# Optimization experiments

Measured on AMD Instinct MI355X. Metric: run time of the kernel, lower is better.

The kernel has to match this reference:

```python
import jax, jax.numpy as jnp
import numpy as np

B, S, D = 1, 4096, 896
NH, NKV, HD = 14, 2, 64
ROPE_BASE = 1000000.0

def rotate_half(x):
    x1, x2 = x[..., :x.shape[-1] // 2], x[..., x.shape[-1] // 2:]
    return jnp.concatenate((-x2, x1), axis=-1)

def rope_tables(seq_len, head_dim, base):
    inv_freq = 1.0 / (base ** (jnp.arange(0, head_dim, 2, dtype=jnp.float32) / head_dim))
    t = jnp.arange(seq_len, dtype=jnp.float32)
    freqs = jnp.einsum('i,j->ij', t, inv_freq)
    emb = jnp.concatenate((freqs, freqs), axis=-1)  # [S, HD]
    return jnp.cos(emb), jnp.sin(emb)

def setup_inputs() -> dict:
    key = jax.random.key(0)
    ks = jax.random.split(key, 6)
    hidden_states = jax.random.normal(ks[0], (B, S, D), dtype=jnp.float32)
    # additive causal mask [1,1,S,S]
    neg = jnp.finfo(jnp.float32).min
    causal = jnp.where(jnp.tril(jnp.ones((S, S), dtype=bool)), 0.0, neg)
    attention_mask = causal[None, None, :, :].astype(jnp.float32)
    sc = 0.02
    Wq = jax.random.normal(ks[1], (D, NH * HD), dtype=jnp.float32) * sc
    Wk = jax.random.normal(ks[2], (D, NKV * HD), dtype=jnp.float32) * sc
    Wv = jax.random.normal(ks[3], (D, NKV * HD), dtype=jnp.float32) * sc
    Wo = jax.random.normal(ks[4], (D, D), dtype=jnp.float32) * sc
    bq = jnp.zeros((NH * HD,), jnp.float32)
    bk = jnp.zeros((NKV * HD,), jnp.float32)
    bv = jnp.zeros((NKV * HD,), jnp.float32)
    return {"hidden_states": hidden_states, "attention_mask": attention_mask,
            "Wq": Wq, "bq": bq, "Wk": Wk, "bk": bk, "Wv": Wv, "bv": bv, "Wo": Wo}

def reference(hidden_states, attention_mask, Wq, bq, Wk, bk, Wv, bv, Wo):
    b, s, _ = hidden_states.shape
    groups = NH // NKV
    q = (hidden_states @ Wq + bq).reshape(b, s, NH, HD)
    k = (hidden_states @ Wk + bk).reshape(b, s, NKV, HD)
    v = (hidden_states @ Wv + bv).reshape(b, s, NKV, HD)
    cos, sin = rope_tables(s, HD, ROPE_BASE)
    cos = cos[None, :, None, :]
    sin = sin[None, :, None, :]
    q = q * cos + rotate_half(q) * sin
    k = k * cos + rotate_half(k) * sin
    # GQA: repeat KV heads
    k = jnp.repeat(k, groups, axis=2)
    v = jnp.repeat(v, groups, axis=2)
    # [b, h, s, d]
    q = jnp.transpose(q, (0, 2, 1, 3))
    k = jnp.transpose(k, (0, 2, 1, 3))
    v = jnp.transpose(v, (0, 2, 1, 3))
    attn = jnp.einsum('bhqd,bhkd->bhqk', q, k) / jnp.sqrt(jnp.float32(HD))
    attn = attn + attention_mask
    attn = jax.nn.softmax(attn, axis=-1)
    out = jnp.einsum('bhqk,bhkd->bhqd', attn, v)
    out = jnp.transpose(out, (0, 2, 1, 3)).reshape(b, s, NH * HD)
    return out @ Wo
```

## Files before the change

### kernel.cpp

```cpp
#include <hip/hip_runtime.h>
#include <math.h>

constexpr int S_    = 4096;
constexpr int Dm    = 896;
constexpr int NHd   = 14;
constexpr int NKVh  = 2;
constexpr int HDim  = 64;
constexpr int NQ    = NHd * HDim;
constexpr int NK    = NKVh * HDim;
constexpr int NQK   = NQ + NK;
constexpr int GROUPS = NHd / NKVh;
constexpr float L2B   = 19.9315685693241740873f;
constexpr float LOG2E = 1.44269504088896340736f;

constexpr int NUNITS = 952;

typedef __attribute__((ext_vector_type(8)))  short bf16x8;
typedef __attribute__((ext_vector_type(4)))  short bf16x4;
typedef __attribute__((ext_vector_type(4)))  float f32x4;
typedef __attribute__((ext_vector_type(16))) float f32x16;
typedef __attribute__((ext_vector_type(4)))  int   i32x4;

__device__ __forceinline__ short f2bf(float f) {
  unsigned u = __builtin_bit_cast(unsigned, f);
  unsigned r = (u + 0x7FFFu + ((u >> 16) & 1u)) >> 16;
  return (short)r;
}
__device__ __forceinline__ float bf2f(short s) {
  return __builtin_bit_cast(float, ((unsigned)(unsigned short)s) << 16);
}

__device__ __forceinline__ unsigned cvtpk(float lo, float hi) {
  unsigned r;
  asm("v_cvt_pk_bf16_f32 %0, %1, %2" : "=v"(r) : "v"(lo), "v"(hi));
  return r;
}

__device__ __forceinline__ void gload16(const void* g, void* l) {
  __builtin_amdgcn_global_load_lds(
      (const __attribute__((address_space(1))) unsigned int*)g,
      (__attribute__((address_space(3))) unsigned int*)l, 16, 0, 0);
}

__global__ __launch_bounds__(256) void prep_all(
    const float* __restrict__ hs, short* __restrict__ hsb,
    float* __restrict__ cost, float* __restrict__ sint,
    const float* __restrict__ Wq, const float* __restrict__ Wk,
    const float* __restrict__ Wv, const float* __restrict__ Wo,
    short* __restrict__ wtq, short* __restrict__ wto)
{
  const int bid = blockIdx.x;
  const int tid = threadIdx.x;
  if (bid < 1792) {
    int idx = bid * 256 + tid;
    float4 a = ((const float4*)hs)[idx * 2];
    float4 b = ((const float4*)hs)[idx * 2 + 1];
    bf16x8 o;
    o[0] = f2bf(a.x); o[1] = f2bf(a.y); o[2] = f2bf(a.z); o[3] = f2bf(a.w);
    o[4] = f2bf(b.x); o[5] = f2bf(b.y); o[6] = f2bf(b.z); o[7] = f2bf(b.w);
    ((bf16x8*)hsb)[idx] = o;
    return;
  }
  if (bid < 2304) {
    int idx = (bid - 1792) * 256 + tid;
    int m = idx >> 5, j = idx & 31;
    float invf = exp2f(-(float)j * (L2B / 32.0f));
    float th = (float)m * invf;
    float s, c;
    sincosf(th, &s, &c);
    cost[idx] = c;
    sint[idx] = s;
    return;
  }
  __shared__ float t[64 * 68];
  const int b2 = bid - 2304;
  const int kt = b2 % 14;
  const int by = b2 / 14;

  const float* src; int srcN, nt; short* dst; int rowOff;
  if (by < 14)      { src = Wq; srcN = NQ; nt = by;      dst = wtq; rowOff = 0; }
  else if (by < 16) { src = Wk; srcN = NK; nt = by - 14; dst = wtq; rowOff = 896; }
  else if (by < 18) { src = Wv; srcN = NK; nt = by - 16; dst = wtq; rowOff = 1024; }
  else              { src = Wo; srcN = NQ; nt = by - 18; dst = wto; rowOff = 0; }

  #pragma unroll
  for (int i = 0; i < 4; i++) {
    int idx = tid + i * 256;
    int r = idx >> 4, c4 = (idx & 15) * 4;
    *(float4*)&t[r * 68 + c4] =
        *(const float4*)&src[(size_t)(kt * 64 + r) * srcN + nt * 64 + c4];
  }
  __syncthreads();
  const int nl = tid >> 2;
  const int kc = (tid & 3) * 16;
  bf16x8 o0, o1;
  #pragma unroll
  for (int i = 0; i < 8; i++) o0[i] = f2bf(t[(kc + i) * 68 + nl]);
  #pragma unroll
  for (int i = 0; i < 8; i++) o1[i] = f2bf(t[(kc + 8 + i) * 68 + nl]);
  short* dp = dst + (size_t)(rowOff + nt * 64 + nl) * 896 + kt * 64 + kc;
  *(bf16x8*)dp = o0;
  *(bf16x8*)(dp + 8) = o1;
}

template<int EPI>
__global__ __launch_bounds__(256) void gemm64(
    const short* __restrict__ A, const short* __restrict__ Bt,
    const float* __restrict__ biasq, const float* __restrict__ biask,
    const float* __restrict__ biasv,
    const float* __restrict__ cost, const float* __restrict__ sint,
    short* __restrict__ qkb, short* __restrict__ vtb,
    float* __restrict__ outp)
{
  __shared__ short Als[64 * 64];
  __shared__ short Bls[128 * 64];
  const int tid = threadIdx.x;
  const int lane = tid & 63;
  const int w = tid >> 6;
  const int wm = w >> 1, wn = w & 1;
  const int r16 = lane & 15, rg = lane >> 4;
  const int bm = blockIdx.x, bn = blockIdx.y;

  const f32x4 zero4 = {0.f, 0.f, 0.f, 0.f};
  f32x4 acc[2][4];
  #pragma unroll
  for (int mt = 0; mt < 2; mt++)
    #pragma unroll
    for (int nt = 0; nt < 4; nt++) acc[mt][nt] = zero4;

  const int srow = (lane >> 3);
  const int scol = (lane & 7) * 8;

  for (int kt = 0; kt < 14; ++kt) {
    __syncthreads();
    #pragma unroll
    for (int i = 0; i < 2; i++) {
      int c = w * 2 + i;
      int row = c * 8 + srow;
      gload16(A + (size_t)(bm * 64 + row) * 896 + kt * 64 + scol, &Als[c * 512]);
    }
    #pragma unroll
    for (int i = 0; i < 4; i++) {
      int c = w * 4 + i;
      int row = c * 8 + srow;
      gload16(Bt + (size_t)(bn * 128 + row) * 896 + kt * 64 + scol, &Bls[c * 512]);
    }
    __syncthreads();

    bf16x8 af[2][2], bfr[4][2];
    #pragma unroll
    for (int mt = 0; mt < 2; mt++)
      #pragma unroll
      for (int ks = 0; ks < 2; ks++)
        af[mt][ks] = *(const bf16x8*)&Als[(wm * 32 + mt * 16 + r16) * 64 + ks * 32 + rg * 8];
    #pragma unroll
    for (int nt = 0; nt < 4; nt++)
      #pragma unroll
      for (int ks = 0; ks < 2; ks++)
        bfr[nt][ks] = *(const bf16x8*)&Bls[(wn * 64 + nt * 16 + r16) * 64 + ks * 32 + rg * 8];
    #pragma unroll
    for (int mt = 0; mt < 2; mt++)
      #pragma unroll
      for (int nt = 0; nt < 4; nt++)
        #pragma unroll
        for (int ks = 0; ks < 2; ks++)
          acc[mt][nt] = __builtin_amdgcn_mfma_f32_16x16x32_bf16(
              af[mt][ks], bfr[nt][ks], acc[mt][nt], 0, 0, 0);
  }

  if (EPI == 0) {
    const int nbase = bn * 128 + wn * 64;
    if (bn < 8) {
      const float scl = (bn < 7) ? (0.125f * LOG2E) : 1.0f;
      const float* bias = (bn < 7) ? biasq : (biask - 896);
      #pragma unroll
      for (int mt = 0; mt < 2; mt++) {
        const int m0 = bm * 64 + wm * 32 + mt * 16 + rg * 4;
        #pragma unroll
        for (int nt = 0; nt < 4; nt++) {
          int n = nbase + nt * 16 + r16;
          int j = n & 31;
          float sgn = (n & 32) ? 1.f : -1.f;
          float b0 = bias[n], b1 = bias[n ^ 32];
          #pragma unroll
          for (int r = 0; r < 4; r++) {
            int m = m0 + r;
            float c_ = cost[m * 32 + j], s_ = sint[m * 32 + j];
            float val = ((acc[mt][nt][r] + b0) * c_ +
                         sgn * (acc[mt][nt ^ 2][r] + b1) * s_) * scl;
            qkb[(size_t)m * NQK + n] = f2bf(val);
          }
        }
      }
    } else {
      #pragma unroll
      for (int mt = 0; mt < 2; mt++) {
        const int m0 = bm * 64 + wm * 32 + mt * 16 + rg * 4;
        #pragma unroll
        for (int nt = 0; nt < 4; nt++) {
          int vc = wn * 64 + nt * 16 + r16;
          float b0 = biasv[vc];
          bf16x4 pk;
          #pragma unroll
          for (int r = 0; r < 4; r++) pk[r] = f2bf(acc[mt][nt][r] + b0);
          *(bf16x4*)&vtb[(size_t)vc * S_ + m0] = pk;
        }
      }
    }
  } else {
    #pragma unroll
    for (int mt = 0; mt < 2; mt++) {
      const int m0 = bm * 64 + wm * 32 + mt * 16 + rg * 4;
      #pragma unroll
      for (int nt = 0; nt < 4; nt++) {
        int n = bn * 128 + wn * 64 + nt * 16 + r16;
        #pragma unroll
        for (int r = 0; r < 4; r++)
          outp[(size_t)(m0 + r) * NQ + n] = acc[mt][nt][r];
      }
    }
  }
}

__global__ __launch_bounds__(256, 3) void flash_mfma(
    const short* __restrict__ qkb, const short* __restrict__ vtb,
    short* __restrict__ attnb, short* __restrict__ orec,
    float* __restrict__ mlrec, unsigned* __restrict__ cnt)
{
  __shared__ __align__(16) char lds[32768];
  __shared__ int s_unit;

  const int tid  = threadIdx.x;
  const int lane = tid & 63;
  const int w    = tid >> 6;
  const int q32  = lane & 31;
  const int hi   = lane >> 5;

  const int c8   = tid & 7;
  const int key0 = tid >> 3;
  const int key1 = key0 + 32;
  const int swz0 = (c8 ^ (key0 & 7)) << 4;
  const int swz1 = (c8 ^ (key1 & 7)) << 4;

  bf16x8 ones;
  #pragma unroll
  for (int j = 0; j < 8; j++) ones[j] = (short)0x3F80;

  for (;;) {
    __syncthreads();
    if (tid == 0) s_unit = (int)atomicAdd(cnt, 1u);
    __syncthreads();
    const int u = s_unit;
    if (u >= NUNITS) break;

    const int e = u / 14;
    const int h = u - e * 14;
    int qt, ci;
    if (e < 36)      { qt = 31 - e / 3; ci = e - (31 - qt) * 3; }
    else if (e < 60) { int f = e - 36; qt = 19 - (f >> 1); ci = f & 1; }
    else             { qt = 67 - e; ci = 0; }
    const int K  = 2 * (qt + 1);
    const int n  = (qt < 8) ? 1 : (qt < 20) ? 2 : 3;
    const int L  = (K + n - 1) / n;
    const int kt_lo = ci * L;
    const int kt_hi = (kt_lo + L < K) ? (kt_lo + L) : K;
    const int kv = h / GROUPS;
    const int q0 = qt * 128;
    const int kbase2 = (NQ + kv * HDim) * 2;
    const int qg = q0 + w * 32 + q32;

    bf16x8 qf[4];
    {
      const short* qp = qkb + (size_t)qg * NQK + h * HDim + hi * 8;
      #pragma unroll
      for (int ks = 0; ks < 4; ++ks) qf[ks] = *(const bf16x8*)(qp + ks * 16);
    }

    f32x16 acc_o[2], acc_l;
    float m_run = 0.f;
    #pragma unroll
    for (int r = 0; r < 16; ++r) { acc_o[0][r] = 0.f; acc_o[1][r] = 0.f; acc_l[r] = 0.f; }

    const char* ksrc0 = (const char*)qkb + (size_t)(kt_lo * 64 + key0) * 2048 + kbase2 + swz0;
    const char* ksrc1 = (const char*)qkb + (size_t)(kt_lo * 64 + key1) * 2048 + kbase2 + swz1;
    const char* vsrc0 = (const char*)vtb + (size_t)(kv * 64 + key0) * 8192 + (size_t)kt_lo * 128 + swz0;
    const char* vsrc1 = (const char*)vtb + (size_t)(kv * 64 + key1) * 8192 + (size_t)kt_lo * 128 + swz1;

    gload16(ksrc0, lds + w * 1024);
    gload16(ksrc1, lds + 4096 + w * 1024);
    gload16(vsrc0, lds + 8192 + w * 1024);
    gload16(vsrc1, lds + 12288 + w * 1024);
    ksrc0 += 131072; ksrc1 += 131072;
    vsrc0 += 128;    vsrc1 += 128;

    for (int kt = kt_lo; kt < kt_hi; ++kt) {
      const int cur = (kt - kt_lo) & 1;
      asm volatile("s_waitcnt vmcnt(0)" ::: "memory");
      __builtin_amdgcn_s_barrier();
      if (kt + 1 < kt_hi) {
        char* B = lds + ((cur ^ 1) << 14);
        gload16(ksrc0, B + w * 1024);
        gload16(ksrc1, B + 4096 + w * 1024);
        gload16(vsrc0, B + 8192 + w * 1024);
        gload16(vsrc1, B + 12288 + w * 1024);
        ksrc0 += 131072; ksrc1 += 131072;
        vsrc0 += 128;    vsrc1 += 128;
      }
      __builtin_amdgcn_sched_barrier(0);
      const char* KsB = lds + (cur << 14);
      const char* VtB = KsB + 8192;
      const int kb = kt * 64;

      f32x16 sc[2];
      #pragma unroll
      for (int r = 0; r < 16; ++r) { sc[0][r] = 0.f; sc[1][r] = 0.f; }
      #pragma unroll
      for (int t = 0; t < 2; ++t) {
        const int key = t * 32 + q32;
        #pragma unroll
        for (int ks = 0; ks < 4; ++ks) {
          bf16x8 kf = *(const bf16x8*)(KsB + key * 128 + (((2 * ks + hi) ^ (key & 7)) << 4));
          sc[t] = __builtin_amdgcn_mfma_f32_32x32x16_bf16(kf, qf[ks], sc[t], 0, 0, 0);
        }
      }

      if (kb + 63 > q0 + w * 32) {
        #pragma unroll
        for (int t = 0; t < 2; ++t)
          #pragma unroll
          for (int r = 0; r < 16; ++r) {
            int key = kb + t * 32 + (r & 3) + 8 * (r >> 2) + 4 * hi;
            sc[t][r] = (key > qg) ? -1e30f : sc[t][r];
          }
      }

      f32x16 mm;
      #pragma unroll
      for (int r = 0; r < 16; ++r) mm[r] = fmaxf(sc[0][r], sc[1][r]);
      #pragma unroll
      for (int r = 0; r < 8; ++r) mm[r] = fmaxf(mm[r], mm[r + 8]);
      #pragma unroll
      for (int r = 0; r < 4; ++r) mm[r] = fmaxf(mm[r], mm[r + 4]);
      float pm = fmaxf(fmaxf(mm[0], mm[1]), fmaxf(mm[2], mm[3]));
      {
        float a = pm, b = pm;
        asm("v_permlane32_swap_b32 %0, %1" : "+v"(a), "+v"(b));
        pm = fmaxf(a, b);
      }

      if (!__all(pm <= m_run + 8.0f)) {
        float newm = fmaxf(m_run, pm);
        float scl = exp2f(m_run - newm);
        m_run = newm;
        acc_l[0] *= scl;
        #pragma unroll
        for (int r = 0; r < 16; ++r) { acc_o[0][r] *= scl; acc_o[1][r] *= scl; }
      }

      #pragma unroll
      for (int t = 0; t < 2; ++t)
        #pragma unroll
        for (int r = 0; r < 16; ++r) sc[t][r] = exp2f(sc[t][r] - m_run);

      unsigned U0[2][4], U1[2][4];
      #pragma unroll
      for (int t = 0; t < 2; ++t)
        #pragma unroll
        for (int a = 0; a < 4; ++a) {
          U0[t][a] = cvtpk(sc[t][4 * a],     sc[t][4 * a + 1]);
          U1[t][a] = cvtpk(sc[t][4 * a + 2], sc[t][4 * a + 3]);
        }

      #pragma unroll
      for (int kp = 0; kp < 4; ++kp) {
        const int t = kp >> 1, c = kp & 1;
        unsigned x0 = U0[t][2 * c], y0 = U0[t][2 * c + 1];
        unsigned x1 = U1[t][2 * c], y1 = U1[t][2 * c + 1];
        asm("v_permlane32_swap_b32 %0, %1" : "+v"(x0), "+v"(y0));
        asm("v_permlane32_swap_b32 %0, %1" : "+v"(x1), "+v"(y1));
        i32x4 pi = {(int)x0, (int)x1, (int)y0, (int)y1};
        bf16x8 pf = __builtin_bit_cast(bf16x8, pi);
        acc_l = __builtin_amdgcn_mfma_f32_32x32x16_bf16(ones, pf, acc_l, 0, 0, 0);
        #pragma unroll
        for (int dt = 0; dt < 2; ++dt) {
          const int d = dt * 32 + q32;
          bf16x8 vf = *(const bf16x8*)(VtB + d * 128 + (((2 * kp + hi) ^ (d & 7)) << 4));
          acc_o[dt] = __builtin_amdgcn_mfma_f32_32x32x16_bf16(vf, pf, acc_o[dt], 0, 0, 0);
        }
      }
    }

    if (n == 1) {
      const float inv = 1.0f / acc_l[0];
      short* op = attnb + (size_t)qg * NQ + h * HDim + 4 * hi;
      #pragma unroll
      for (int dt = 0; dt < 2; ++dt)
        #pragma unroll
        for (int rq = 0; rq < 4; ++rq) {
          bf16x4 pk;
          pk[0] = f2bf(acc_o[dt][4 * rq]     * inv);
          pk[1] = f2bf(acc_o[dt][4 * rq + 1] * inv);
          pk[2] = f2bf(acc_o[dt][4 * rq + 2] * inv);
          pk[3] = f2bf(acc_o[dt][4 * rq + 3] * inv);
          *(bf16x4*)(op + dt * 32 + 8 * rq) = pk;
        }
    } else {
      const int qloc = w * 32 + q32;
      short* op;
      if (ci == 0) {
        op = attnb + (size_t)qg * NQ + h * HDim + 4 * hi;
      } else {
        int er = (qt < 20) ? (h * 36 + (qt - 8))
                           : (h * 36 + 12 + (qt - 20) * 2 + (ci - 1));
        op = orec + (size_t)er * 8192 + (size_t)qloc * 64 + 4 * hi;
      }
      #pragma unroll
      for (int dt = 0; dt < 2; ++dt)
        #pragma unroll
        for (int rq = 0; rq < 4; ++rq) {
          bf16x4 pk;
          pk[0] = f2bf(acc_o[dt][4 * rq]);
          pk[1] = f2bf(acc_o[dt][4 * rq + 1]);
          pk[2] = f2bf(acc_o[dt][4 * rq + 2]);
          pk[3] = f2bf(acc_o[dt][4 * rq + 3]);
          *(bf16x4*)(op + dt * 32 + 8 * rq) = pk;
        }
      if (hi == 0) {
        int co = (qt < 20) ? (8 + (qt - 8) * 2 + ci) : (32 + (qt - 20) * 3 + ci);
        float2 ml = {m_run, acc_l[0]};
        *(float2*)(mlrec + ((size_t)(h * 68 + co) * 128 + qloc) * 2) = ml;
      }
    }
  }
}

__global__ __launch_bounds__(128) void merge_chunks(
    const short* __restrict__ orec, const float* __restrict__ mlrec,
    short* __restrict__ attnb)
{
  const int b = blockIdx.x;
  const int h = b / 24;
  const int qt = 8 + (b - h * 24);
  const int n = (qt < 20) ? 2 : 3;
  const int qloc = threadIdx.x;
  const int q = qt * 128 + qloc;

  const int co0 = (qt < 20) ? (8 + (qt - 8) * 2) : (32 + (qt - 20) * 3);
  float2 ml0 = *(const float2*)(mlrec + ((size_t)(h * 68 + co0)     * 128 + qloc) * 2);
  float2 ml1 = *(const float2*)(mlrec + ((size_t)(h * 68 + co0 + 1) * 128 + qloc) * 2);
  float2 ml2 = (n == 3)
      ? *(const float2*)(mlrec + ((size_t)(h * 68 + co0 + 2) * 128 + qloc) * 2)
      : float2{-3.0e38f, 0.f};

  float M = fmaxf(fmaxf(ml0.x, ml1.x), ml2.x);
  float a0 = exp2f(ml0.x - M), a1 = exp2f(ml1.x - M);
  float a2 = (n == 3) ? exp2f(ml2.x - M) : 0.f;
  float inv = 1.0f / (a0 * ml0.y + a1 * ml1.y + a2 * ml2.y);
  float s0 = a0 * inv, s1 = a1 * inv, s2 = a2 * inv;

  const int er1 = (qt < 20) ? (h * 36 + (qt - 8)) : (h * 36 + 12 + (qt - 20) * 2);
  short* O0 = attnb + (size_t)q * NQ + h * HDim;
  const short* O1 = orec + (size_t)er1 * 8192 + (size_t)qloc * 64;
  const short* O2 = (n == 3) ? (O1 + 8192) : O1;

  #pragma unroll
  for (int i = 0; i < 8; i++) {
    bf16x8 x0 = *(const bf16x8*)(O0 + i * 8);
    bf16x8 x1 = *(const bf16x8*)(O1 + i * 8);
    bf16x8 x2 = *(const bf16x8*)(O2 + i * 8);
    bf16x8 o;
    #pragma unroll
    for (int j = 0; j < 8; j++)
      o[j] = f2bf(s0 * bf2f(x0[j]) + s1 * bf2f(x1[j]) + s2 * bf2f(x2[j]));
    *(bf16x8*)(O0 + i * 8) = o;
  }
}

extern "C" void kernel_launch(void* const* d_in, const int* in_sizes, int n_in,
                              void* d_out, int out_size, void* d_ws, size_t ws_size,
                              hipStream_t stream)
{
  const float* hs = (const float*)d_in[0];
  const float* Wq = (const float*)d_in[2];
  const float* bq = (const float*)d_in[3];
  const float* Wk = (const float*)d_in[4];
  const float* bk = (const float*)d_in[5];
  const float* Wv = (const float*)d_in[6];
  const float* bv = (const float*)d_in[7];
  const float* Wo = (const float*)d_in[8];

  short* hsb  = (short*)d_ws;
  short* wtq  = hsb + (size_t)S_ * Dm;
  short* wto  = wtq + (size_t)1152 * 896;
  float* cost = (float*)(wto + (size_t)896 * 896);
  float* sint = cost + (size_t)S_ * 32;
  short* qkb  = (short*)(sint + (size_t)S_ * 32);
  short* vtb  = qkb + (size_t)S_ * NQK;
  short* attnb= vtb + (size_t)NK * S_;
  float* out  = (float*)d_out;

  short*    orec  = hsb;
  float*    mlrec = cost;
  unsigned* cnt   = (unsigned*)((char*)attnb + (size_t)S_ * NQ * 2);

  hipLaunchKernelGGL(prep_all, dim3(2752), dim3(256), 0, stream,
                     hs, hsb, cost, sint, Wq, Wk, Wv, Wo, wtq, wto);
  hipLaunchKernelGGL((gemm64<0>), dim3(64, 9), dim3(256), 0, stream,
                     hsb, wtq, bq, bk, bv, cost, sint, qkb, vtb, (float*)nullptr);
  hipMemsetAsync(cnt, 0, 4, stream);
  hipLaunchKernelGGL(flash_mfma, dim3(768), dim3(256), 0, stream,
                     qkb, vtb, attnb, orec, mlrec, cnt);
  hipLaunchKernelGGL(merge_chunks, dim3(336), dim3(128), 0, stream,
                     orec, mlrec, attnb);
  hipLaunchKernelGGL((gemm64<1>), dim3(64, 7), dim3(256), 0, stream,
                     attnb, wto, bq, bk, bv, cost, sint,
                     (short*)nullptr, (short*)nullptr, out);
}
```

Before: 131.8 us.

## Enlarge flash attention query tile to 256 rows with 8-wave blocks

Doubles the query tile per work unit from 128 to 256 rows by using 512-thread blocks (8 waves). Each K/V tile loaded into LDS is now shared by twice as many queries, which halves K/V global traffic per query and halves the per-thread load count. The split-KV chunk schedule, the partial-result buffers (now split across two workspace regions) and the merge kernel are reworked to handle up to 4 chunks per query tile. In exchange there are fewer, larger units, so load balancing is coarser, and the 512-thread launch bound with 4 blocks per CU may restrict registers.

```diff
diff --git a/kernel.cpp b/kernel.cpp
--- a/kernel.cpp
+++ b/kernel.cpp
@@ -13,7 +13,7 @@
 constexpr float L2B   = 19.9315685693241740873f;
 constexpr float LOG2E = 1.44269504088896340736f;
 
-constexpr int NUNITS = 952;
+constexpr int NUNITS = 560;
 
 typedef __attribute__((ext_vector_type(8)))  short bf16x8;
 typedef __attribute__((ext_vector_type(4)))  short bf16x4;
@@ -222,10 +222,11 @@
   }
 }
 
-__global__ __launch_bounds__(256, 3) void flash_mfma(
+__global__ __launch_bounds__(512, 4) void flash_mfma(
     const short* __restrict__ qkb, const short* __restrict__ vtb,
-    short* __restrict__ attnb, short* __restrict__ orec,
-    float* __restrict__ mlrec, unsigned* __restrict__ cnt)
+    short* __restrict__ attnb, short* __restrict__ orec1,
+    short* __restrict__ orec2, float* __restrict__ mlrec,
+    unsigned* __restrict__ cnt)
 {
   __shared__ __align__(16) char lds[32768];
   __shared__ int s_unit;
@@ -236,11 +237,9 @@
   const int q32  = lane & 31;
   const int hi   = lane >> 5;
 
-  const int c8   = tid & 7;
-  const int key0 = tid >> 3;
-  const int key1 = key0 + 32;
-  const int swz0 = (c8 ^ (key0 & 7)) << 4;
-  const int swz1 = (c8 ^ (key1 & 7)) << 4;
+  const int key = tid >> 3;
+  const int c8  = tid & 7;
+  const int swz = (c8 ^ (key & 7)) << 4;
 
   bf16x8 ones;
   #pragma unroll
@@ -255,17 +254,17 @@
 
     const int e = u / 14;
     const int h = u - e * 14;
-    int qt, ci;
-    if (e < 36)      { qt = 31 - e / 3; ci = e - (31 - qt) * 3; }
-    else if (e < 60) { int f = e - 36; qt = 19 - (f >> 1); ci = f & 1; }
-    else             { qt = 67 - e; ci = 0; }
-    const int K  = 2 * (qt + 1);
-    const int n  = (qt < 8) ? 1 : (qt < 20) ? 2 : 3;
+    int qt, ci, n;
+    if (e < 16)      { qt = 15 - (e >> 2); ci = e & 3; n = 4; }
+    else if (e < 28) { int f = e - 16; qt = 11 - f / 3; ci = f - 3 * (f / 3); n = 3; }
+    else if (e < 36) { int f = e - 28; qt = 7 - (f >> 1); ci = f & 1; n = 2; }
+    else             { qt = 39 - e; ci = 0; n = 1; }
+    const int K  = 4 * (qt + 1);
     const int L  = (K + n - 1) / n;
     const int kt_lo = ci * L;
     const int kt_hi = (kt_lo + L < K) ? (kt_lo + L) : K;
     const int kv = h / GROUPS;
-    const int q0 = qt * 128;
+    const int q0 = qt * 256;
     const int kbase2 = (NQ + kv * HDim) * 2;
     const int qg = q0 + w * 32 + q32;
 
@@ -281,17 +280,13 @@
     #pragma unroll
     for (int r = 0; r < 16; ++r) { acc_o[0][r] = 0.f; acc_o[1][r] = 0.f; acc_l[r] = 0.f; }
 
-    const char* ksrc0 = (const char*)qkb + (size_t)(kt_lo * 64 + key0) * 2048 + kbase2 + swz0;
-    const char* ksrc1 = (const char*)qkb + (size_t)(kt_lo * 64 + key1) * 2048 + kbase2 + swz1;
-    const char* vsrc0 = (const char*)vtb + (size_t)(kv * 64 + key0) * 8192 + (size_t)kt_lo * 128 + swz0;
-    const char* vsrc1 = (const char*)vtb + (size_t)(kv * 64 + key1) * 8192 + (size_t)kt_lo * 128 + swz1;
-
-    gload16(ksrc0, lds + w * 1024);
-    gload16(ksrc1, lds + 4096 + w * 1024);
-    gload16(vsrc0, lds + 8192 + w * 1024);
-    gload16(vsrc1, lds + 12288 + w * 1024);
-    ksrc0 += 131072; ksrc1 += 131072;
-    vsrc0 += 128;    vsrc1 += 128;
+    const char* ksrc = (const char*)qkb + (size_t)(kt_lo * 64 + key) * 2048 + kbase2 + swz;
+    const char* vsrc = (const char*)vtb + (size_t)(kv * 64 + key) * 8192 + (size_t)kt_lo * 128 + swz;
+
+    gload16(ksrc, lds + w * 1024);
+    gload16(vsrc, lds + 8192 + w * 1024);
+    ksrc += 131072;
+    vsrc += 128;
 
     for (int kt = kt_lo; kt < kt_hi; ++kt) {
       const int cur = (kt - kt_lo) & 1;
@@ -299,12 +294,10 @@
       __builtin_amdgcn_s_barrier();
       if (kt + 1 < kt_hi) {
         char* B = lds + ((cur ^ 1) << 14);
-        gload16(ksrc0, B + w * 1024);
-        gload16(ksrc1, B + 4096 + w * 1024);
-        gload16(vsrc0, B + 8192 + w * 1024);
-        gload16(vsrc1, B + 12288 + w * 1024);
-        ksrc0 += 131072; ksrc1 += 131072;
-        vsrc0 += 128;    vsrc1 += 128;
+        gload16(ksrc, B + w * 1024);
+        gload16(vsrc, B + 8192 + w * 1024);
+        ksrc += 131072;
+        vsrc += 128;
       }
       __builtin_amdgcn_sched_barrier(0);
       const char* KsB = lds + (cur << 14);
@@ -316,10 +309,10 @@
       for (int r = 0; r < 16; ++r) { sc[0][r] = 0.f; sc[1][r] = 0.f; }
       #pragma unroll
       for (int t = 0; t < 2; ++t) {
-        const int key = t * 32 + q32;
+        const int krow = t * 32 + q32;
         #pragma unroll
         for (int ks = 0; ks < 4; ++ks) {
-          bf16x8 kf = *(const bf16x8*)(KsB + key * 128 + (((2 * ks + hi) ^ (key & 7)) << 4));
+          bf16x8 kf = *(const bf16x8*)(KsB + krow * 128 + (((2 * ks + hi) ^ (krow & 7)) << 4));
           sc[t] = __builtin_amdgcn_mfma_f32_32x32x16_bf16(kf, qf[ks], sc[t], 0, 0, 0);
         }
       }
@@ -329,8 +322,8 @@
         for (int t = 0; t < 2; ++t)
           #pragma unroll
           for (int r = 0; r < 16; ++r) {
-            int key = kb + t * 32 + (r & 3) + 8 * (r >> 2) + 4 * hi;
-            sc[t][r] = (key > qg) ? -1e30f : sc[t][r];
+            int kg = kb + t * 32 + (r & 3) + 8 * (r >> 2) + 4 * hi;
+            sc[t][r] = (kg > qg) ? -1e30f : sc[t][r];
           }
       }
 
@@ -410,9 +403,13 @@
       if (ci == 0) {
         op = attnb + (size_t)qg * NQ + h * HDim + 4 * hi;
       } else {
-        int er = (qt < 20) ? (h * 36 + (qt - 8))
-                           : (h * 36 + 12 + (qt - 20) * 2 + (ci - 1));
-        op = orec + (size_t)er * 8192 + (size_t)qloc * 64 + 4 * hi;
+        int er = (qt < 8) ? (qt - 4)
+               : (qt < 12) ? (4 + (qt - 8) * 2 + (ci - 1))
+                           : (12 + (qt - 12) * 3 + (ci - 1));
+        int er_g = h * 24 + er;
+        short* ob = (er_g < 287) ? (orec1 + (size_t)er_g * 16384)
+                                 : (orec2 + (size_t)(er_g - 287) * 16384);
+        op = ob + (size_t)qloc * 64 + 4 * hi;
       }
       #pragma unroll
       for (int dt = 0; dt < 2; ++dt)
@@ -426,52 +423,75 @@
           *(bf16x4*)(op + dt * 32 + 8 * rq) = pk;
         }
       if (hi == 0) {
-        int co = (qt < 20) ? (8 + (qt - 8) * 2 + ci) : (32 + (qt - 20) * 3 + ci);
+        int co = (qt < 8) ? ((qt - 4) * 2 + ci)
+               : (qt < 12) ? (8 + (qt - 8) * 3 + ci)
+                           : (20 + (qt - 12) * 4 + ci);
         float2 ml = {m_run, acc_l[0]};
-        *(float2*)(mlrec + ((size_t)(h * 68 + co) * 128 + qloc) * 2) = ml;
-      }
-    }
-  }
-}
-
-__global__ __launch_bounds__(128) void merge_chunks(
-    const short* __restrict__ orec, const float* __restrict__ mlrec,
-    short* __restrict__ attnb)
+        *(float2*)(mlrec + ((size_t)(h * 36 + co) * 256 + qloc) * 2) = ml;
+      }
+    }
+  }
+}
+
+__global__ __launch_bounds__(256) void merge_chunks(
+    const short* __restrict__ orec1, const short* __restrict__ orec2,
+    const float* __restrict__ mlrec, short* __restrict__ attnb)
 {
   const int b = blockIdx.x;
-  const int h = b / 24;
-  const int qt = 8 + (b - h * 24);
-  const int n = (qt < 20) ? 2 : 3;
+  const int h = b / 12;
+  const int qt = 4 + (b - h * 12);
+  const int n = (qt < 8) ? 2 : (qt < 12) ? 3 : 4;
   const int qloc = threadIdx.x;
-  const int q = qt * 128 + qloc;
-
-  const int co0 = (qt < 20) ? (8 + (qt - 8) * 2) : (32 + (qt - 20) * 3);
-  float2 ml0 = *(const float2*)(mlrec + ((size_t)(h * 68 + co0)     * 128 + qloc) * 2);
-  float2 ml1 = *(const float2*)(mlrec + ((size_t)(h * 68 + co0 + 1) * 128 + qloc) * 2);
-  float2 ml2 = (n == 3)
-      ? *(const float2*)(mlrec + ((size_t)(h * 68 + co0 + 2) * 128 + qloc) * 2)
-      : float2{-3.0e38f, 0.f};
-
-  float M = fmaxf(fmaxf(ml0.x, ml1.x), ml2.x);
-  float a0 = exp2f(ml0.x - M), a1 = exp2f(ml1.x - M);
-  float a2 = (n == 3) ? exp2f(ml2.x - M) : 0.f;
-  float inv = 1.0f / (a0 * ml0.y + a1 * ml1.y + a2 * ml2.y);
-  float s0 = a0 * inv, s1 = a1 * inv, s2 = a2 * inv;
-
-  const int er1 = (qt < 20) ? (h * 36 + (qt - 8)) : (h * 36 + 12 + (qt - 20) * 2);
+  const int q = qt * 256 + qloc;
+
+  const int co0 = (qt < 8) ? ((qt - 4) * 2)
+                : (qt < 12) ? (8 + (qt - 8) * 3)
+                            : (20 + (qt - 12) * 4);
+  const int er0 = (qt < 8) ? (qt - 4)
+                : (qt < 12) ? (4 + (qt - 8) * 2)
+                            : (12 + (qt - 12) * 3);
+  const int er0_g = h * 24 + er0;
+
+  float2 ml[4];
+  #pragma unroll
+  for (int ci = 0; ci < 4; ci++)
+    ml[ci] = (ci < n)
+        ? *(const float2*)(mlrec + ((size_t)(h * 36 + co0 + ci) * 256 + qloc) * 2)
+        : float2{-3.0e38f, 0.f};
+
+  float M = fmaxf(fmaxf(ml[0].x, ml[1].x), fmaxf(ml[2].x, ml[3].x));
+  float s[4];
+  float lsum = 0.f;
+  #pragma unroll
+  for (int ci = 0; ci < 4; ci++) {
+    s[ci] = (ci < n) ? exp2f(ml[ci].x - M) : 0.f;
+    lsum += s[ci] * ml[ci].y;
+  }
+  float inv = 1.0f / lsum;
+  #pragma unroll
+  for (int ci = 0; ci < 4; ci++) s[ci] *= inv;
+
   short* O0 = attnb + (size_t)q * NQ + h * HDim;
-  const short* O1 = orec + (size_t)er1 * 8192 + (size_t)qloc * 64;
-  const short* O2 = (n == 3) ? (O1 + 8192) : O1;
+  const short* Op[3];
+  #pragma unroll
+  for (int ci = 1; ci < 4; ci++) {
+    int eg = er0_g + (ci - 1);
+    const short* ob = (eg < 287) ? (orec1 + (size_t)eg * 16384)
+                                 : (orec2 + (size_t)(eg - 287) * 16384);
+    Op[ci - 1] = ob + (size_t)qloc * 64;
+  }
 
   #pragma unroll
   for (int i = 0; i < 8; i++) {
     bf16x8 x0 = *(const bf16x8*)(O0 + i * 8);
-    bf16x8 x1 = *(const bf16x8*)(O1 + i * 8);
-    bf16x8 x2 = *(const bf16x8*)(O2 + i * 8);
+    bf16x8 x1 = *(const bf16x8*)(Op[0] + i * 8);
+    bf16x8 x2 = (n >= 3) ? *(const bf16x8*)(Op[1] + i * 8) : x1;
+    bf16x8 x3 = (n >= 4) ? *(const bf16x8*)(Op[2] + i * 8) : x1;
     bf16x8 o;
     #pragma unroll
     for (int j = 0; j < 8; j++)
-      o[j] = f2bf(s0 * bf2f(x0[j]) + s1 * bf2f(x1[j]) + s2 * bf2f(x2[j]));
+      o[j] = f2bf(s[0] * bf2f(x0[j]) + s[1] * bf2f(x1[j]) +
+                  s[2] * bf2f(x2[j]) + s[3] * bf2f(x3[j]));
     *(bf16x8*)(O0 + i * 8) = o;
   }
 }
@@ -499,19 +519,20 @@
   short* attnb= vtb + (size_t)NK * S_;
   float* out  = (float*)d_out;
 
-  short*    orec  = hsb;
+  short*    orec1 = hsb;
   float*    mlrec = cost;
   unsigned* cnt   = (unsigned*)((char*)attnb + (size_t)S_ * NQ * 2);
+  short*    orec2 = (short*)((char*)cnt + 4096);
 
   hipLaunchKernelGGL(prep_all, dim3(2752), dim3(256), 0, stream,
                      hs, hsb, cost, sint, Wq, Wk, Wv, Wo, wtq, wto);
   hipLaunchKernelGGL((gemm64<0>), dim3(64, 9), dim3(256), 0, stream,
                      hsb, wtq, bq, bk, bv, cost, sint, qkb, vtb, (float*)nullptr);
   hipMemsetAsync(cnt, 0, 4, stream);
-  hipLaunchKernelGGL(flash_mfma, dim3(768), dim3(256), 0, stream,
-                     qkb, vtb, attnb, orec, mlrec, cnt);
-  hipLaunchKernelGGL(merge_chunks, dim3(336), dim3(128), 0, stream,
-                     orec, mlrec, attnb);
+  hipLaunchKernelGGL(flash_mfma, dim3(512), dim3(512), 0, stream,
+                     qkb, vtb, attnb, orec1, orec2, mlrec, cnt);
+  hipLaunchKernelGGL(merge_chunks, dim3(168), dim3(256), 0, stream,
+                     orec1, orec2, mlrec, attnb);
   hipLaunchKernelGGL((gemm64<1>), dim3(64, 7), dim3(256), 0, stream,
                      attnb, wto, bq, bk, bv, cost, sint,
                      (short*)nullptr, (short*)nullptr, out);
```

After: 144.7 us. +9.8%, slower.
